# Optimization experiments

Measured on AMD Instinct MI355X. Metric: run time of the kernel, lower is better.

Reference implementation:

```python
import jax, jax.numpy as jnp
import numpy as np


def setup_inputs() -> dict:
    key = jax.random.key(0)
    ks = jax.random.split(key, 5)
    b, t, q_dim, kv_dim, h = 16, 128, 256, 64, 4
    c = t - 1
    q_x = jax.random.normal(ks[0], (b, t, q_dim), dtype=jnp.float32)
    kv_x = jax.random.normal(ks[1], (b, t, c, kv_dim), dtype=jnp.float32)
    # Linear weights stored as [in, out]; no biases (bias=False in torch module).
    sq = 1.0 / np.sqrt(q_dim)
    sk = 1.0 / np.sqrt(kv_dim)
    Wq = jax.random.uniform(ks[2], (q_dim, kv_dim * h), jnp.float32, -sq, sq)
    Wk = jax.random.uniform(ks[3], (kv_dim, kv_dim * h), jnp.float32, -sk, sk)
    Wv = jax.random.uniform(ks[4], (kv_dim, kv_dim * h), jnp.float32, -sk, sk)
    return {"q_x": q_x, "kv_x": kv_x, "Wq": Wq, "Wk": Wk, "Wv": Wv}


def reference(q_x, kv_x, Wq, Wk, Wv):
    b, t, c, k = kv_x.shape  # c = t - 1
    h = Wq.shape[1] // k
    # projections
    q = (q_x @ Wq).reshape(b, t, h, k)          # [b,t,h,k]
    keys = (kv_x @ Wk).reshape(b, t, c, h, k)   # [b,t,c,h,k]
    vals = (kv_x @ Wv).reshape(b, t, c, h, k)
    # per-token attention over the c-sized context
    scores = jnp.einsum('bthk,btchk->bthc', q, keys) / jnp.sqrt(jnp.float32(k))
    w = jax.nn.softmax(scores, axis=-1)          # softmax over context dim
    out = jnp.einsum('bthc,btchk->bthk', w, vals)
    return out.reshape(b, t, h * k)
```

## Files before the change

kernel.cpp:

```cpp
#include <hip/hip_runtime.h>
#include <math.h>

#define Bdim 16
#define Tdim 128
#define Cdim 127
#define Hdim 4
#define QD   256
#define HK   256
#define BT   (Bdim * Tdim)

#define DPP_XOR1 0xB1
#define DPP_XOR2 0x4E
template<int CTRL>
__device__ __forceinline__ float dpp_movf(float x) {
    return __int_as_float(__builtin_amdgcn_update_dpp(
        0, __float_as_int(x), CTRL, 0xF, 0xF, true));
}
__device__ __forceinline__ float dot4(float4 a, float4 b, float s) {
    return fmaf(a.x, b.x, fmaf(a.y, b.y, fmaf(a.z, b.z, fmaf(a.w, b.w, s))));
}
__device__ __forceinline__ float4 fma4(float e, float4 x, float4 v) {
    v.x = fmaf(e, x.x, v.x); v.y = fmaf(e, x.y, v.y);
    v.z = fmaf(e, x.z, v.z); v.w = fmaf(e, x.w, v.w);
    return v;
}
__device__ __forceinline__ float4 add4(float4 a, float4 b) {
    return make_float4(a.x + b.x, a.y + b.y, a.z + b.z, a.w + b.w);
}
__device__ __forceinline__ float4 shfl4(float4 v, int m) {
    return make_float4(__shfl_xor(v.x, m, 64), __shfl_xor(v.y, m, 64),
                       __shfl_xor(v.z, m, 64), __shfl_xor(v.w, m, 64));
}
__device__ __forceinline__ float4 sel4(int c, float4 a, float4 b) {
    return c ? a : b;
}

__global__ __launch_bounds__(256) void qk_fused(
        const float* __restrict__ q_x,
        const float* __restrict__ Wq,
        const float* __restrict__ Wk,
        float* __restrict__ qk) {
    __shared__ __align__(16) float q_s[4][256];
    __shared__ __align__(16) float p_s[4][4][68];
    int RB = blockIdx.x;
    int tid = threadIdx.x;
    {
        int r = tid >> 6, kq = tid & 63;
        *(float4*)&q_s[r][kq*4] =
            *(const float4*)(q_x + (size_t)(RB*4 + r) * QD + kq * 4);
    }
    __syncthreads();

    float acc[4] = {0.f, 0.f, 0.f, 0.f};
    #pragma unroll 4
    for (int i4 = 0; i4 < 64; ++i4) {
        float w0 = Wq[(size_t)(4*i4+0) * HK + tid];
        float w1 = Wq[(size_t)(4*i4+1) * HK + tid];
        float w2 = Wq[(size_t)(4*i4+2) * HK + tid];
        float w3 = Wq[(size_t)(4*i4+3) * HK + tid];
        #pragma unroll
        for (int r = 0; r < 4; ++r) {
            float4 qv = *(const float4*)&q_s[r][i4*4];
            acc[r] = fmaf(qv.x, w0, fmaf(qv.y, w1, fmaf(qv.z, w2, fmaf(qv.w, w3, acc[r]))));
        }
    }
    int h = tid >> 6, m = tid & 63;
    #pragma unroll
    for (int r = 0; r < 4; ++r) p_s[r][h][m] = acc[r];
    __syncthreads();

    const float4* wk4 = (const float4*)(Wk + (size_t)m * HK + h * 64);
    float4 wkr[16];
    #pragma unroll
    for (int j = 0; j < 16; ++j) wkr[j] = wk4[j];
    float a2[4] = {0.f, 0.f, 0.f, 0.f};
    #pragma unroll
    for (int j4 = 0; j4 < 16; ++j4) {
        #pragma unroll
        for (int r = 0; r < 4; ++r) {
            float4 pv = *(const float4*)&p_s[r][h][j4*4];
            a2[r] = fmaf(pv.x, wkr[j4].x, fmaf(pv.y, wkr[j4].y,
                    fmaf(pv.z, wkr[j4].z, fmaf(pv.w, wkr[j4].w, a2[r]))));
        }
    }
    #pragma unroll
    for (int r = 0; r < 4; ++r)
        qk[(size_t)(RB*4 + r) * HK + tid] = a2[r];
}

__global__ __launch_bounds__(256, 2) void attn_fused(
        const float* __restrict__ kv_x,
        const float* __restrict__ qk_g,
        const float* __restrict__ Wv,
        float* __restrict__ out) {
    __shared__ __align__(16) float4 wx_s[4][64];
    int tid = threadIdx.x;
    int wv = tid >> 6, lane = tid & 63;
    int bt = blockIdx.x * 4 + wv;
    int r  = lane >> 2;
    int jq = lane & 3;
    const float* Xr = kv_x + (size_t)bt * (Cdim * 64);

    const float4* qb = (const float4*)(qk_g + (size_t)bt * HK);
    float4 Q00 = qb[ 0 + jq*4 + 0], Q01 = qb[ 0 + jq*4 + 1],
           Q02 = qb[ 0 + jq*4 + 2], Q03 = qb[ 0 + jq*4 + 3];
    float4 Q10 = qb[16 + jq*4 + 0], Q11 = qb[16 + jq*4 + 1],
           Q12 = qb[16 + jq*4 + 2], Q13 = qb[16 + jq*4 + 3];
    float4 Q20 = qb[32 + jq*4 + 0], Q21 = qb[32 + jq*4 + 1],
           Q22 = qb[32 + jq*4 + 2], Q23 = qb[32 + jq*4 + 3];
    float4 Q30 = qb[48 + jq*4 + 0], Q31 = qb[48 + jq*4 + 1],
           Q32 = qb[48 + jq*4 + 2], Q33 = qb[48 + jq*4 + 3];

    float4 V00={0,0,0,0},V01={0,0,0,0},V02={0,0,0,0},V03={0,0,0,0};
    float4 V10={0,0,0,0},V11={0,0,0,0},V12={0,0,0,0},V13={0,0,0,0};
    float4 V20={0,0,0,0},V21={0,0,0,0},V22={0,0,0,0},V23={0,0,0,0};
    float4 V30={0,0,0,0},V31={0,0,0,0},V32={0,0,0,0},V33={0,0,0,0};
    float d0=0.f, d1=0.f, d2=0.f, d3=0.f;
    float4 A0, A1, A2, A3, B0, B1, B2, B3, C0, C1, C2, C3;

#define LOADR(P0,P1,P2,P3,KK) do {                                           \
    int c_ = 16*(KK) + r;                                                    \
    const float4* xp_ = (const float4*)(Xr + (size_t)((c_ < Cdim) ? c_ : 0)  \
                                        * 64) + jq * 4;                      \
    P0 = xp_[0]; P1 = xp_[1]; P2 = xp_[2]; P3 = xp_[3];                      \
} while (0)

#define COMP(P0,P1,P2,P3,KK) do {                                            \
    float s0 = dot4(Q00,P0,0.f); s0 = dot4(Q01,P1,s0);                       \
    s0 = dot4(Q02,P2,s0); s0 = dot4(Q03,P3,s0);                              \
    float s1 = dot4(Q10,P0,0.f); s1 = dot4(Q11,P1,s1);                       \
    s1 = dot4(Q12,P2,s1); s1 = dot4(Q13,P3,s1);                              \
    float s2 = dot4(Q20,P0,0.f); s2 = dot4(Q21,P1,s2);                       \
    s2 = dot4(Q22,P2,s2); s2 = dot4(Q23,P3,s2);                              \
    float s3 = dot4(Q30,P0,0.f); s3 = dot4(Q31,P1,s3);                       \
    s3 = dot4(Q32,P2,s3); s3 = dot4(Q33,P3,s3);                              \
    s0 += dpp_movf<DPP_XOR1>(s0); s0 += dpp_movf<DPP_XOR2>(s0);              \
    s1 += dpp_movf<DPP_XOR1>(s1); s1 += dpp_movf<DPP_XOR2>(s1);              \
    s2 += dpp_movf<DPP_XOR1>(s2); s2 += dpp_movf<DPP_XOR2>(s2);              \
    s3 += dpp_movf<DPP_XOR1>(s3); s3 += dpp_movf<DPP_XOR2>(s3);              \
    bool vld_ = (16*(KK) + r) < Cdim;                                        \
    float e0 = vld_ ? __expf(s0 * 0.125f) : 0.f;                             \
    float e1 = vld_ ? __expf(s1 * 0.125f) : 0.f;                             \
    float e2 = vld_ ? __expf(s2 * 0.125f) : 0.f;                             \
    float e3 = vld_ ? __expf(s3 * 0.125f) : 0.f;                             \
    d0 += e0; d1 += e1; d2 += e2; d3 += e3;                                  \
    V00=fma4(e0,P0,V00); V01=fma4(e0,P1,V01);                                \
    V02=fma4(e0,P2,V02); V03=fma4(e0,P3,V03);                                \
    V10=fma4(e1,P0,V10); V11=fma4(e1,P1,V11);                                \
    V12=fma4(e1,P2,V12); V13=fma4(e1,P3,V13);                                \
    V20=fma4(e2,P0,V20); V21=fma4(e2,P1,V21);                                \
    V22=fma4(e2,P2,V22); V23=fma4(e2,P3,V23);                                \
    V30=fma4(e3,P0,V30); V31=fma4(e3,P1,V31);                                \
    V32=fma4(e3,P2,V32); V33=fma4(e3,P3,V33);                                \
} while (0)

    LOADR(A0,A1,A2,A3,0);
    LOADR(B0,B1,B2,B3,1);
    LOADR(C0,C1,C2,C3,2);
    COMP (A0,A1,A2,A3,0);
    LOADR(A0,A1,A2,A3,3);
    COMP (B0,B1,B2,B3,1);
    LOADR(B0,B1,B2,B3,4);
    COMP (C0,C1,C2,C3,2);
    LOADR(C0,C1,C2,C3,5);
    COMP (A0,A1,A2,A3,3);
    LOADR(A0,A1,A2,A3,6);
    COMP (B0,B1,B2,B3,4);
    LOADR(B0,B1,B2,B3,7);
    COMP (C0,C1,C2,C3,5);
    COMP (A0,A1,A2,A3,6);
    COMP (B0,B1,B2,B3,7);
#undef LOADR
#undef COMP

    int r0 = (lane >> 2) & 1, r1 = (lane >> 3) & 1;
    int r2 = (lane >> 4) & 1, r3 = (lane >> 5) & 1;
    float4 K00 = add4(sel4(r0, V01, V00), shfl4(sel4(r0, V00, V01), 4));
    float4 K01 = add4(sel4(r0, V03, V02), shfl4(sel4(r0, V02, V03), 4));
    float4 K10 = add4(sel4(r0, V11, V10), shfl4(sel4(r0, V10, V11), 4));
    float4 K11 = add4(sel4(r0, V13, V12), shfl4(sel4(r0, V12, V13), 4));
    float4 K20 = add4(sel4(r0, V21, V20), shfl4(sel4(r0, V20, V21), 4));
    float4 K21 = add4(sel4(r0, V23, V22), shfl4(sel4(r0, V22, V23), 4));
    float4 K30 = add4(sel4(r0, V31, V30), shfl4(sel4(r0, V30, V31), 4));
    float4 K31 = add4(sel4(r0, V33, V32), shfl4(sel4(r0, V32, V33), 4));
    float4 L0 = add4(sel4(r1, K01, K00), shfl4(sel4(r1, K00, K01), 8));
    float4 L1 = add4(sel4(r1, K11, K10), shfl4(sel4(r1, K10, K11), 8));
    float4 L2 = add4(sel4(r1, K21, K20), shfl4(sel4(r1, K20, K21), 8));
    float4 L3 = add4(sel4(r1, K31, K30), shfl4(sel4(r1, K30, K31), 8));
    float4 M0 = add4(sel4(r2, L1, L0), shfl4(sel4(r2, L0, L1), 16));
    float4 M1 = add4(sel4(r2, L3, L2), shfl4(sel4(r2, L2, L3), 16));
    float4 F = add4(sel4(r3, M1, M0), shfl4(sel4(r3, M0, M1), 32));

    #pragma unroll
    for (int m = 4; m <= 32; m <<= 1) {
        d0 += __shfl_xor(d0, m, 64); d1 += __shfl_xor(d1, m, 64);
        d2 += __shfl_xor(d2, m, 64); d3 += __shfl_xor(d3, m, 64);
    }

    int H  = (r3 << 1) | r2;
    int qo = (r1 << 1) | r0;
    wx_s[wv][H * 16 + jq * 4 + qo] = F;

    {
        float inv0 = 1.f / d0, inv1 = 1.f / d1, inv2 = 1.f / d2, inv3 = 1.f / d3;
        float* obt = out + (size_t)bt * HK;
        #pragma unroll
        for (int p = 0; p < 4; ++p) {
            const float* wvc = Wv + p * 64 + lane;
            float acc = 0.f;
            #pragma unroll
            for (int j4 = 0; j4 < 16; ++j4) {
                float4 w4 = wx_s[wv][p * 16 + j4];
                acc = fmaf(w4.x, wvc[(size_t)(j4*4+0) * HK],
                      fmaf(w4.y, wvc[(size_t)(j4*4+1) * HK],
                      fmaf(w4.z, wvc[(size_t)(j4*4+2) * HK],
                      fmaf(w4.w, wvc[(size_t)(j4*4+3) * HK], acc))));
            }
            float inv = (p == 0) ? inv0 : (p == 1) ? inv1
                      : (p == 2) ? inv2 : inv3;
            obt[p * 64 + lane] = acc * inv;
        }
    }
}

extern "C" void kernel_launch(void* const* d_in, const int* in_sizes, int n_in,
                              void* d_out, int out_size, void* d_ws, size_t ws_size,
                              hipStream_t stream) {
    const float* q_x  = (const float*)d_in[0];
    const float* kv_x = (const float*)d_in[1];
    const float* Wq   = (const float*)d_in[2];
    const float* Wk   = (const float*)d_in[3];
    const float* Wv   = (const float*)d_in[4];
    float* out = (float*)d_out;

    float* qk = (float*)d_ws;

    qk_fused <<<BT / 4, 256, 0, stream>>>(q_x, Wq, Wk, qk);
    attn_fused<<<BT / 4, 256, 0, stream>>>(kv_x, qk, Wv, out);
}
```

Before: 36.62 us.

## Split attention heads across wave pairs to halve per-wave register state

Each (b,t) row is now handled by two waves, each owning two of the four heads. This halves the per-wave accumulators and Q registers, reduces the load pipeline from triple to double buffering, and raises the launch-bounds occupancy hint. The final Wv projection is done block-wide after a shared-memory exchange and a __syncthreads. The cost is that every kv_x row is loaded twice (once per head-pair wave), with an added barrier and twice as many blocks.

```diff
diff --git a/kernel.cpp b/kernel.cpp
--- a/kernel.cpp
+++ b/kernel.cpp
@@ -88,35 +88,32 @@
         qk[(size_t)(RB*4 + r) * HK + tid] = a2[r];
 }
 
-__global__ __launch_bounds__(256, 2) void attn_fused(
+__global__ __launch_bounds__(256, 4) void attn_fused(
         const float* __restrict__ kv_x,
         const float* __restrict__ qk_g,
         const float* __restrict__ Wv,
         float* __restrict__ out) {
-    __shared__ __align__(16) float4 wx_s[4][64];
+    __shared__ __align__(16) float4 wx_s[2][4][16];
+    __shared__ float dn_s[2][4];
     int tid = threadIdx.x;
     int wv = tid >> 6, lane = tid & 63;
-    int bt = blockIdx.x * 4 + wv;
+    int slot = wv >> 1;
+    int hp   = wv & 1;
+    int bt = blockIdx.x * 2 + slot;
     int r  = lane >> 2;
     int jq = lane & 3;
     const float* Xr = kv_x + (size_t)bt * (Cdim * 64);
 
     const float4* qb = (const float4*)(qk_g + (size_t)bt * HK);
-    float4 Q00 = qb[ 0 + jq*4 + 0], Q01 = qb[ 0 + jq*4 + 1],
-           Q02 = qb[ 0 + jq*4 + 2], Q03 = qb[ 0 + jq*4 + 3];
-    float4 Q10 = qb[16 + jq*4 + 0], Q11 = qb[16 + jq*4 + 1],
-           Q12 = qb[16 + jq*4 + 2], Q13 = qb[16 + jq*4 + 3];
-    float4 Q20 = qb[32 + jq*4 + 0], Q21 = qb[32 + jq*4 + 1],
-           Q22 = qb[32 + jq*4 + 2], Q23 = qb[32 + jq*4 + 3];
-    float4 Q30 = qb[48 + jq*4 + 0], Q31 = qb[48 + jq*4 + 1],
-           Q32 = qb[48 + jq*4 + 2], Q33 = qb[48 + jq*4 + 3];
+    float4 Q00 = qb[(2*hp+0)*16 + jq*4 + 0], Q01 = qb[(2*hp+0)*16 + jq*4 + 1],
+           Q02 = qb[(2*hp+0)*16 + jq*4 + 2], Q03 = qb[(2*hp+0)*16 + jq*4 + 3];
+    float4 Q10 = qb[(2*hp+1)*16 + jq*4 + 0], Q11 = qb[(2*hp+1)*16 + jq*4 + 1],
+           Q12 = qb[(2*hp+1)*16 + jq*4 + 2], Q13 = qb[(2*hp+1)*16 + jq*4 + 3];
 
     float4 V00={0,0,0,0},V01={0,0,0,0},V02={0,0,0,0},V03={0,0,0,0};
     float4 V10={0,0,0,0},V11={0,0,0,0},V12={0,0,0,0},V13={0,0,0,0};
-    float4 V20={0,0,0,0},V21={0,0,0,0},V22={0,0,0,0},V23={0,0,0,0};
-    float4 V30={0,0,0,0},V31={0,0,0,0},V32={0,0,0,0},V33={0,0,0,0};
-    float d0=0.f, d1=0.f, d2=0.f, d3=0.f;
-    float4 A0, A1, A2, A3, B0, B1, B2, B3, C0, C1, C2, C3;
+    float d0=0.f, d1=0.f;
+    float4 A0, A1, A2, A3, B0, B1, B2, B3;
 
 #define LOADR(P0,P1,P2,P3,KK) do {                                           \
     int c_ = 16*(KK) + r;                                                    \
@@ -130,44 +127,32 @@
     s0 = dot4(Q02,P2,s0); s0 = dot4(Q03,P3,s0);                              \
     float s1 = dot4(Q10,P0,0.f); s1 = dot4(Q11,P1,s1);                       \
     s1 = dot4(Q12,P2,s1); s1 = dot4(Q13,P3,s1);                              \
-    float s2 = dot4(Q20,P0,0.f); s2 = dot4(Q21,P1,s2);                       \
-    s2 = dot4(Q22,P2,s2); s2 = dot4(Q23,P3,s2);                              \
-    float s3 = dot4(Q30,P0,0.f); s3 = dot4(Q31,P1,s3);                       \
-    s3 = dot4(Q32,P2,s3); s3 = dot4(Q33,P3,s3);                              \
     s0 += dpp_movf<DPP_XOR1>(s0); s0 += dpp_movf<DPP_XOR2>(s0);              \
     s1 += dpp_movf<DPP_XOR1>(s1); s1 += dpp_movf<DPP_XOR2>(s1);              \
-    s2 += dpp_movf<DPP_XOR1>(s2); s2 += dpp_movf<DPP_XOR2>(s2);              \
-    s3 += dpp_movf<DPP_XOR1>(s3); s3 += dpp_movf<DPP_XOR2>(s3);              \
     bool vld_ = (16*(KK) + r) < Cdim;                                        \
     float e0 = vld_ ? __expf(s0 * 0.125f) : 0.f;                             \
     float e1 = vld_ ? __expf(s1 * 0.125f) : 0.f;                             \
-    float e2 = vld_ ? __expf(s2 * 0.125f) : 0.f;                             \
-    float e3 = vld_ ? __expf(s3 * 0.125f) : 0.f;                             \
-    d0 += e0; d1 += e1; d2 += e2; d3 += e3;                                  \
+    d0 += e0; d1 += e1;                                                      \
     V00=fma4(e0,P0,V00); V01=fma4(e0,P1,V01);                                \
     V02=fma4(e0,P2,V02); V03=fma4(e0,P3,V03);                                \
     V10=fma4(e1,P0,V10); V11=fma4(e1,P1,V11);                                \
     V12=fma4(e1,P2,V12); V13=fma4(e1,P3,V13);                                \
-    V20=fma4(e2,P0,V20); V21=fma4(e2,P1,V21);                                \
-    V22=fma4(e2,P2,V22); V23=fma4(e2,P3,V23);                                \
-    V30=fma4(e3,P0,V30); V31=fma4(e3,P1,V31);                                \
-    V32=fma4(e3,P2,V32); V33=fma4(e3,P3,V33);                                \
 } while (0)
 
     LOADR(A0,A1,A2,A3,0);
     LOADR(B0,B1,B2,B3,1);
-    LOADR(C0,C1,C2,C3,2);
     COMP (A0,A1,A2,A3,0);
-    LOADR(A0,A1,A2,A3,3);
+    LOADR(A0,A1,A2,A3,2);
     COMP (B0,B1,B2,B3,1);
-    LOADR(B0,B1,B2,B3,4);
-    COMP (C0,C1,C2,C3,2);
-    LOADR(C0,C1,C2,C3,5);
-    COMP (A0,A1,A2,A3,3);
+    LOADR(B0,B1,B2,B3,3);
+    COMP (A0,A1,A2,A3,2);
+    LOADR(A0,A1,A2,A3,4);
+    COMP (B0,B1,B2,B3,3);
+    LOADR(B0,B1,B2,B3,5);
+    COMP (A0,A1,A2,A3,4);
     LOADR(A0,A1,A2,A3,6);
-    COMP (B0,B1,B2,B3,4);
+    COMP (B0,B1,B2,B3,5);
     LOADR(B0,B1,B2,B3,7);
-    COMP (C0,C1,C2,C3,5);
     COMP (A0,A1,A2,A3,6);
     COMP (B0,B1,B2,B3,7);
 #undef LOADR
@@ -179,47 +164,39 @@
     float4 K01 = add4(sel4(r0, V03, V02), shfl4(sel4(r0, V02, V03), 4));
     float4 K10 = add4(sel4(r0, V11, V10), shfl4(sel4(r0, V10, V11), 4));
     float4 K11 = add4(sel4(r0, V13, V12), shfl4(sel4(r0, V12, V13), 4));
-    float4 K20 = add4(sel4(r0, V21, V20), shfl4(sel4(r0, V20, V21), 4));
-    float4 K21 = add4(sel4(r0, V23, V22), shfl4(sel4(r0, V22, V23), 4));
-    float4 K30 = add4(sel4(r0, V31, V30), shfl4(sel4(r0, V30, V31), 4));
-    float4 K31 = add4(sel4(r0, V33, V32), shfl4(sel4(r0, V32, V33), 4));
     float4 L0 = add4(sel4(r1, K01, K00), shfl4(sel4(r1, K00, K01), 8));
     float4 L1 = add4(sel4(r1, K11, K10), shfl4(sel4(r1, K10, K11), 8));
-    float4 L2 = add4(sel4(r1, K21, K20), shfl4(sel4(r1, K20, K21), 8));
-    float4 L3 = add4(sel4(r1, K31, K30), shfl4(sel4(r1, K30, K31), 8));
-    float4 M0 = add4(sel4(r2, L1, L0), shfl4(sel4(r2, L0, L1), 16));
-    float4 M1 = add4(sel4(r2, L3, L2), shfl4(sel4(r2, L2, L3), 16));
-    float4 F = add4(sel4(r3, M1, M0), shfl4(sel4(r3, M0, M1), 32));
+    float4 M = add4(sel4(r2, L1, L0), shfl4(sel4(r2, L0, L1), 16));
+    float4 F = add4(M, shfl4(M, 32));
 
     #pragma unroll
     for (int m = 4; m <= 32; m <<= 1) {
-        d0 += __shfl_xor(d0, m, 64); d1 += __shfl_xor(d1, m, 64);
-        d2 += __shfl_xor(d2, m, 64); d3 += __shfl_xor(d3, m, 64);
-    }
-
-    int H  = (r3 << 1) | r2;
+        d0 += __shfl_xor(d0, m, 64);
+        d1 += __shfl_xor(d1, m, 64);
+    }
+
+    int H  = 2*hp + r2;
     int qo = (r1 << 1) | r0;
-    wx_s[wv][H * 16 + jq * 4 + qo] = F;
-
-    {
-        float inv0 = 1.f / d0, inv1 = 1.f / d1, inv2 = 1.f / d2, inv3 = 1.f / d3;
-        float* obt = out + (size_t)bt * HK;
+    if (r3 == 0) wx_s[slot][H][jq * 4 + qo] = F;
+    if (lane == 0) { dn_s[slot][2*hp+0] = d0; dn_s[slot][2*hp+1] = d1; }
+    __syncthreads();
+
+    #pragma unroll
+    for (int s = 0; s < 2; ++s) {
+        int col = tid;
+        int h = col >> 6;
+        float inv = 1.f / dn_s[s][h];
+        const float* wvc = Wv + col;
+        float acc = 0.f;
         #pragma unroll
-        for (int p = 0; p < 4; ++p) {
-            const float* wvc = Wv + p * 64 + lane;
-            float acc = 0.f;
-            #pragma unroll
-            for (int j4 = 0; j4 < 16; ++j4) {
-                float4 w4 = wx_s[wv][p * 16 + j4];
-                acc = fmaf(w4.x, wvc[(size_t)(j4*4+0) * HK],
-                      fmaf(w4.y, wvc[(size_t)(j4*4+1) * HK],
-                      fmaf(w4.z, wvc[(size_t)(j4*4+2) * HK],
-                      fmaf(w4.w, wvc[(size_t)(j4*4+3) * HK], acc))));
-            }
-            float inv = (p == 0) ? inv0 : (p == 1) ? inv1
-                      : (p == 2) ? inv2 : inv3;
-            obt[p * 64 + lane] = acc * inv;
+        for (int j4 = 0; j4 < 16; ++j4) {
+            float4 w4 = wx_s[s][h][j4];
+            acc = fmaf(w4.x, wvc[(size_t)(j4*4+0) * HK],
+                  fmaf(w4.y, wvc[(size_t)(j4*4+1) * HK],
+                  fmaf(w4.z, wvc[(size_t)(j4*4+2) * HK],
+                  fmaf(w4.w, wvc[(size_t)(j4*4+3) * HK], acc))));
         }
+        out[(size_t)(blockIdx.x * 2 + s) * HK + col] = acc * inv;
     }
 }
 
@@ -236,5 +213,5 @@
     float* qk = (float*)d_ws;
 
     qk_fused <<<BT / 4, 256, 0, stream>>>(q_x, Wq, Wk, qk);
-    attn_fused<<<BT / 4, 256, 0, stream>>>(kv_x, qk, Wv, out);
-}
+    attn_fused<<<BT / 2, 256, 0, stream>>>(kv_x, qk, Wv, out);
+}
```

Measured after the change: 36.00 us (median of 2 runs). About the same (-1.7%).
